# Performance work log

Hardware: AMD Instinct MI355X
Metric: run time of the kernel (lower is better)

Reference implementation:

```python
import jax, jax.numpy as jnp
import numpy as np

NUM_USERS = 100000
NUM_ITEMS = 50000
N_NODES = NUM_USERS + NUM_ITEMS
LATENT_DIM = 64
N_LAYERS = 3
N_EDGES = 4800000


def setup_inputs() -> dict:
    key = jax.random.key(0)
    ks = jax.random.split(key, 7)
    user_emb = jax.random.normal(ks[0], (NUM_USERS, LATENT_DIM), dtype=jnp.float32) * 0.1
    item_emb = jax.random.normal(ks[1], (NUM_ITEMS, LATENT_DIM), dtype=jnp.float32) * 0.1
    edge_src = jax.random.randint(ks[2], (N_EDGES,), 0, N_NODES, dtype=jnp.int32)
    edge_dst = jax.random.randint(ks[3], (N_EDGES,), 0, N_NODES, dtype=jnp.int32)
    # normalized adjacency values (positive, ~1/deg scale)
    edge_vals = jax.random.uniform(ks[4], (N_EDGES,), dtype=jnp.float32) * 0.05
    users = jax.random.randint(ks[5], (1024,), 0, NUM_USERS, dtype=jnp.int32)
    items = jax.random.randint(ks[6], (20000,), 0, NUM_ITEMS, dtype=jnp.int32)
    return {"user_emb": user_emb, "item_emb": item_emb,
            "edge_src": edge_src, "edge_dst": edge_dst, "edge_vals": edge_vals,
            "users": users, "items": items}


def _spmm(edge_src, edge_dst, edge_vals, x):
    # y[dst] += vals * x[src]  == sparse.mm(Graph, x)
    msgs = edge_vals[:, None] * x[edge_src]           # [E, D]
    return jax.ops.segment_sum(msgs, edge_dst, num_segments=N_NODES)


def reference(user_emb, item_emb, edge_src, edge_dst, edge_vals, users, items):
    all_em = jnp.concatenate([user_emb, item_emb], axis=0)  # [N, D]
    acc = all_em  # running sum over layers (mean at the end)
    h = all_em
    for _ in range(N_LAYERS):
        h = _spmm(edge_src, edge_dst, edge_vals, h)
        acc = acc + h
    result = acc / jnp.float32(N_LAYERS + 1)  # mean over stacked layers
    all_users = result[:NUM_USERS]
    all_items = result[NUM_USERS:]
    u = all_users[users]        # [Bu, D]
    it = all_items[items]       # [Bi, D]
    ratings = jax.nn.sigmoid(jnp.matmul(u, it.T))  # [Bu, Bi]
    return ratings
```

## Files before the change

### kernel.cpp

```cpp
#include <hip/hip_runtime.h>
#include <hip/hip_bf16.h>

#define NUM_USERS 100000
#define NUM_ITEMS 50000
#define N_NODES   150000
#define DIM       64
#define N_LAYERS  3
#define N_QU      1024
#define N_QI      20000
#define N_QTOT    (N_QU + N_QI)
#define SLOTS     80

#define BIN_SHIFT 9
#define BIN_W     512
#define NBINS     ((N_NODES + BIN_W - 1) >> BIN_SHIFT)
#define BIN_CAP   17472
#define S1_BATCH  4096

typedef __attribute__((ext_vector_type(8))) short bf16x8;
typedef __attribute__((ext_vector_type(4))) float f32x4;
typedef __attribute__((ext_vector_type(8))) unsigned short u16x8;

__device__ __forceinline__ short f2bf(float x) {
    unsigned u = __float_as_uint(x);
    u += 0x7FFF + ((u >> 16) & 1);
    return (short)(u >> 16);
}
__device__ __forceinline__ float bf2f(unsigned short u) {
    return __uint_as_float((unsigned)u << 16);
}

__global__ void init_h0(const float* __restrict__ ue, const float* __restrict__ ie,
                        unsigned short* __restrict__ h0) {
    const size_t n8   = (size_t)N_NODES * DIM / 8;
    const size_t uend = (size_t)NUM_USERS * DIM / 8;
    size_t stride = (size_t)gridDim.x * blockDim.x;
    for (size_t i = (size_t)blockIdx.x * blockDim.x + threadIdx.x; i < n8; i += stride) {
        const float4* s = (i < uend) ? ((const float4*)ue) + i * 2
                                     : ((const float4*)ie) + (i - uend) * 2;
        float4 a = s[0], b = s[1];
        ushort4 lo, hi;
        lo.x = (unsigned short)f2bf(a.x); lo.y = (unsigned short)f2bf(a.y);
        lo.z = (unsigned short)f2bf(a.z); lo.w = (unsigned short)f2bf(a.w);
        hi.x = (unsigned short)f2bf(b.x); hi.y = (unsigned short)f2bf(b.y);
        hi.z = (unsigned short)f2bf(b.z); hi.w = (unsigned short)f2bf(b.w);
        ((ushort4*)h0)[i * 2]     = lo;
        ((ushort4*)h0)[i * 2 + 1] = hi;
    }
}

__global__ void build_qlist(const int* __restrict__ users, const int* __restrict__ items,
                            int* __restrict__ qlist) {
    int i = blockIdx.x * blockDim.x + threadIdx.x;
    if (i < N_QU) qlist[i] = users[i];
    else if (i < N_QTOT) qlist[i] = NUM_USERS + items[i - N_QU];
}

__global__ __launch_bounds__(256) void s1_coarse(
        const int* __restrict__ src, const int* __restrict__ dst,
        const float* __restrict__ vals, int* __restrict__ gcnt,
        int2* __restrict__ binned, int n) {
    __shared__ int2 staging[S1_BATCH];
    __shared__ int  hist[NBINS];
    __shared__ int  base[NBINS];
    __shared__ int  pfx[NBINS];
    __shared__ int  part[256];
    const int t  = threadIdx.x;
    const int b0 = blockIdx.x * S1_BATCH;
    const int n4 = n >> 2;
    const int i4base = b0 >> 2;
    const int4*   d4 = (const int4*)dst;
    const int4*   s4 = (const int4*)src;
    const float4* v4 = (const float4*)vals;

    for (int i = t; i < NBINS; i += 256) hist[i] = 0;
    __syncthreads();

    #pragma unroll
    for (int k = 0; k < 4; ++k) {
        int i4 = i4base + k * 256 + t;
        if (i4 < n4) {
            int4 d = d4[i4];
            atomicAdd(&hist[d.x >> BIN_SHIFT], 1);
            atomicAdd(&hist[d.y >> BIN_SHIFT], 1);
            atomicAdd(&hist[d.z >> BIN_SHIFT], 1);
            atomicAdd(&hist[d.w >> BIN_SHIFT], 1);
        }
    }
    for (int e = (n & ~3) + t; e < n; e += 256)
        if (e >= b0 && e < b0 + S1_BATCH)
            atomicAdd(&hist[dst[e] >> BIN_SHIFT], 1);
    __syncthreads();

    {
        int i0 = 2 * t, i1 = 2 * t + 1;
        int h0v = (i0 < NBINS) ? hist[i0] : 0;
        int h1v = (i1 < NBINS) ? hist[i1] : 0;
        int s = h0v + h1v;
        part[t] = s;
        __syncthreads();
        int x = s;
        for (int off = 1; off < 256; off <<= 1) {
            int y = (t >= off) ? part[t - off] : 0;
            __syncthreads();
            x += y;
            part[t] = x;
            __syncthreads();
        }
        int exc = x - s;
        if (i0 < NBINS) pfx[i0] = exc;
        if (i1 < NBINS) pfx[i1] = exc + h0v;
    }
    __syncthreads();

    for (int i = t; i < NBINS; i += 256) {
        int c = hist[i];
        base[i] = (c > 0) ? atomicAdd(&gcnt[i], c) : 0;
    }
    __syncthreads();
    for (int i = t; i < NBINS; i += 256) hist[i] = 0;
    __syncthreads();

    #pragma unroll
    for (int k = 0; k < 4; ++k) {
        int i4 = i4base + k * 256 + t;
        if (i4 < n4) {
            int4   d = d4[i4];
            int4   s = s4[i4];
            float4 v = v4[i4];
            int bin, loc;
            bin = d.x >> BIN_SHIFT; loc = atomicAdd(&hist[bin], 1);
            staging[pfx[bin] + loc] = make_int2(((d.x & (BIN_W-1)) << 18) | s.x, __float_as_int(v.x));
            bin = d.y >> BIN_SHIFT; loc = atomicAdd(&hist[bin], 1);
            staging[pfx[bin] + loc] = make_int2(((d.y & (BIN_W-1)) << 18) | s.y, __float_as_int(v.y));
            bin = d.z >> BIN_SHIFT; loc = atomicAdd(&hist[bin], 1);
            staging[pfx[bin] + loc] = make_int2(((d.z & (BIN_W-1)) << 18) | s.z, __float_as_int(v.z));
            bin = d.w >> BIN_SHIFT; loc = atomicAdd(&hist[bin], 1);
            staging[pfx[bin] + loc] = make_int2(((d.w & (BIN_W-1)) << 18) | s.w, __float_as_int(v.w));
        }
    }
    for (int e = (n & ~3) + t; e < n; e += 256)
        if (e >= b0 && e < b0 + S1_BATCH) {
            int d = dst[e];
            int bin = d >> BIN_SHIFT;
            int loc = atomicAdd(&hist[bin], 1);
            staging[pfx[bin] + loc] = make_int2(((d & (BIN_W-1)) << 18) | src[e], __float_as_int(vals[e]));
        }
    __syncthreads();

    {
        int wid = t >> 6, lane = t & 63;
        for (int bin = wid; bin < NBINS; bin += 4) {
            int c = hist[bin];
            int g = base[bin];
            int p = pfx[bin];
            for (int l = lane; l < c; l += 64) {
                int slot = g + l;
                if (slot < BIN_CAP)
                    binned[(size_t)bin * BIN_CAP + slot] = staging[p + l];
            }
        }
    }
}

__global__ __launch_bounds__(1024) void s2_fine(
        const int* __restrict__ gcnt, const int2* __restrict__ binned,
        int* __restrict__ cnt, int2* __restrict__ buckets) {
    __shared__ int cursor[BIN_W];
    const int bin = blockIdx.x;
    const int t   = threadIdx.x;
    if (t < BIN_W) cursor[t] = 0;
    __syncthreads();

    int m = gcnt[bin]; if (m > BIN_CAP) m = BIN_CAP;
    const int2* bp = &binned[(size_t)bin * BIN_CAP];
    for (int i = t; i < m; i += 1024) {
        int2 p  = bp[i];
        int  dl = ((unsigned)p.x) >> 18;
        int  local = atomicAdd(&cursor[dl], 1);
        if (local < SLOTS) {
            int node = (bin << BIN_SHIFT) + dl;
            buckets[(size_t)node * SLOTS + local] =
                make_int2(p.x & 0x3FFFF, p.y);
        }
    }
    __syncthreads();

    if (t < BIN_W) {
        int node = (bin << BIN_SHIFT) + t;
        if (node < N_NODES) {
            int c = cursor[t]; if (c > SLOTS) c = SLOTS;
            cnt[node] = c;
        }
    }
}

__global__ __launch_bounds__(256) void spmm_bucket_bf16(
        const int* __restrict__ cnt, const int2* __restrict__ buckets,
        const unsigned short* __restrict__ x, unsigned short* __restrict__ y,
        const int* __restrict__ list, int count) {
    int lane8   = threadIdx.x & 7;
    int group   = (int)((blockIdx.x * blockDim.x + threadIdx.x) >> 3);
    int ngroups = (int)((gridDim.x * blockDim.x) >> 3);
    const u16x8* x8 = (const u16x8*)x;

    int i = group;
    if (i >= count) return;
    int node_n = list ? list[i] : i;
    int m_n = cnt[node_n];

    for (; i < count; i += ngroups) {
        int node = node_n;
        int m = m_n; if (m > SLOTS) m = SLOTS;
        int j = i + ngroups;
        if (j < count) { node_n = list ? list[j] : j; m_n = cnt[node_n]; }

        const int2* row  = &buckets[(size_t)node * SLOTS];
        const int4* row2 = (const int4*)row;
        float r[8];
        #pragma unroll
        for (int k = 0; k < 8; ++k) r[k] = 0.0f;

        int e = 0;
        for (; e + 4 <= m; e += 4) {
            int4 pa = row2[(e >> 1)];
            int4 pb = row2[(e >> 1) + 1];
            u16x8 x0 = x8[(size_t)pa.x * 8 + lane8];
            u16x8 x1 = x8[(size_t)pa.z * 8 + lane8];
            u16x8 x2 = x8[(size_t)pb.x * 8 + lane8];
            u16x8 x3 = x8[(size_t)pb.z * 8 + lane8];
            float v0 = __int_as_float(pa.y), v1 = __int_as_float(pa.w);
            float v2 = __int_as_float(pb.y), v3 = __int_as_float(pb.w);
            #pragma unroll
            for (int k = 0; k < 8; ++k) r[k] += v0 * bf2f(x0[k]);
            #pragma unroll
            for (int k = 0; k < 8; ++k) r[k] += v1 * bf2f(x1[k]);
            #pragma unroll
            for (int k = 0; k < 8; ++k) r[k] += v2 * bf2f(x2[k]);
            #pragma unroll
            for (int k = 0; k < 8; ++k) r[k] += v3 * bf2f(x3[k]);
        }
        if (e + 2 <= m) {
            int4 pa = row2[(e >> 1)];
            u16x8 x0 = x8[(size_t)pa.x * 8 + lane8];
            u16x8 x1 = x8[(size_t)pa.z * 8 + lane8];
            float v0 = __int_as_float(pa.y), v1 = __int_as_float(pa.w);
            #pragma unroll
            for (int k = 0; k < 8; ++k) r[k] += v0 * bf2f(x0[k]);
            #pragma unroll
            for (int k = 0; k < 8; ++k) r[k] += v1 * bf2f(x1[k]);
            e += 2;
        }
        if (e < m) {
            int2 p = row[e];
            float v = __int_as_float(p.y);
            u16x8 x0 = x8[(size_t)p.x * 8 + lane8];
            #pragma unroll
            for (int k = 0; k < 8; ++k) r[k] += v * bf2f(x0[k]);
        }

        u16x8 o;
        #pragma unroll
        for (int k = 0; k < 8; ++k) o[k] = (unsigned short)f2bf(r[k]);
        ((u16x8*)y)[(size_t)node * 8 + lane8] = o;
    }
}

__global__ __launch_bounds__(256) void prep_packed(
        const float* __restrict__ ue, const float* __restrict__ ie,
        const unsigned short* __restrict__ h1, const unsigned short* __restrict__ h2,
        const unsigned short* __restrict__ h3, const int* __restrict__ users,
        const int* __restrict__ items, unsigned short* __restrict__ packed) {
    int idx = blockIdx.x * blockDim.x + threadIdx.x;
    if (idx >= N_QTOT * 8) return;
    int q = idx >> 3, lane = idx & 7;

    const float* e0;
    size_t hoff;
    if (q < N_QU) {
        int u = users[q];
        e0   = &ue[(size_t)u * DIM];
        hoff = (size_t)u * DIM;
    } else {
        int it = items[q - N_QU];
        e0   = &ie[(size_t)it * DIM];
        hoff = (size_t)(NUM_USERS + it) * DIM;
    }
    int d0 = lane * 8;
    const float4* s0 = (const float4*)&e0[d0];
    float4 a0 = s0[0], a1 = s0[1];
    u16x8 b1 = *(const u16x8*)&h1[hoff + d0];
    u16x8 b2 = *(const u16x8*)&h2[hoff + d0];
    u16x8 b3 = *(const u16x8*)&h3[hoff + d0];

    float v[8];
    v[0] = a0.x; v[1] = a0.y; v[2] = a0.z; v[3] = a0.w;
    v[4] = a1.x; v[5] = a1.y; v[6] = a1.z; v[7] = a1.w;
    u16x8 o;
    #pragma unroll
    for (int k = 0; k < 8; ++k) {
        float t = (v[k] + bf2f(b1[k]) + bf2f(b2[k]) + bf2f(b3[k])) * 0.25f;
        o[k] = (unsigned short)f2bf(t);
    }
    *(u16x8*)&packed[(size_t)q * DIM + d0] = o;
}

__global__ __launch_bounds__(256) void rating_mfma(
        const unsigned short* __restrict__ packed, float* __restrict__ out) {
    __shared__ short Ut[64 * 72];
    __shared__ short Tt[256 * 72];
    const int bj = blockIdx.x;
    const int bi = blockIdx.y;
    const int tid = threadIdx.x;

    {
        int r = tid >> 2, c16 = (tid & 3) * 16;
        const bf16x8* s = (const bf16x8*)&packed[(size_t)(bi * 64 + r) * DIM + c16];
        *(bf16x8*)&Ut[r * 72 + c16]     = s[0];
        *(bf16x8*)&Ut[r * 72 + c16 + 8] = s[1];
    }

    #pragma unroll
    for (int p = 0; p < 4; ++p) {
        int r = (tid >> 2) + p * 64, c16 = (tid & 3) * 16;
        int jg = bj * 256 + r;
        bf16x8 lo = (bf16x8)(short)0, hi = (bf16x8)(short)0;
        if (jg < N_QI) {
            const bf16x8* s = (const bf16x8*)&packed[(size_t)(N_QU + jg) * DIM + c16];
            lo = s[0]; hi = s[1];
        }
        *(bf16x8*)&Tt[r * 72 + c16]     = lo;
        *(bf16x8*)&Tt[r * 72 + c16 + 8] = hi;
    }
    __syncthreads();

    const int wv = tid >> 6, lane = tid & 63;
    const int lr = lane & 15, kq = lane >> 4;

    f32x4 c[4][4];
    #pragma unroll
    for (int mr = 0; mr < 4; ++mr)
        #pragma unroll
        for (int nr = 0; nr < 4; ++nr)
            c[mr][nr] = (f32x4)(0.0f);

    #pragma unroll
    for (int kb = 0; kb < 2; ++kb) {
        bf16x8 a[4], b[4];
        #pragma unroll
        for (int mr = 0; mr < 4; ++mr)
            a[mr] = *(const bf16x8*)&Ut[(mr * 16 + lr) * 72 + (kb * 4 + kq) * 8];
        #pragma unroll
        for (int nr = 0; nr < 4; ++nr)
            b[nr] = *(const bf16x8*)&Tt[(wv * 64 + nr * 16 + lr) * 72 + (kb * 4 + kq) * 8];
        #pragma unroll
        for (int mr = 0; mr < 4; ++mr)
            #pragma unroll
            for (int nr = 0; nr < 4; ++nr)
                c[mr][nr] = __builtin_amdgcn_mfma_f32_16x16x32_bf16(a[mr], b[nr], c[mr][nr], 0, 0, 0);
    }

    #pragma unroll
    for (int mr = 0; mr < 4; ++mr) {
        int rowg = bi * 64 + mr * 16 + kq * 4;
        #pragma unroll
        for (int nr = 0; nr < 4; ++nr) {
            int colg = bj * 256 + wv * 64 + nr * 16 + lr;
            if (colg < N_QI) {
                #pragma unroll
                for (int q = 0; q < 4; ++q) {
                    float z = c[mr][nr][q];
                    out[(size_t)(rowg + q) * N_QI + colg] = 1.0f / (1.0f + __expf(-z));
                }
            }
        }
    }
}

extern "C" void kernel_launch(void* const* d_in, const int* in_sizes, int n_in,
                              void* d_out, int out_size, void* d_ws, size_t ws_size,
                              hipStream_t stream) {
    const float* user_emb  = (const float*)d_in[0];
    const float* item_emb  = (const float*)d_in[1];
    const int*   edge_src  = (const int*)d_in[2];
    const int*   edge_dst  = (const int*)d_in[3];
    const float* edge_vals = (const float*)d_in[4];
    const int*   users     = (const int*)d_in[5];
    const int*   items     = (const int*)d_in[6];
    float*       out       = (float*)d_out;
    int n_edges = in_sizes[2];

    const size_t nodeElems = (size_t)N_NODES * DIM;

    unsigned short* h0 = (unsigned short*)d_ws;
    unsigned short* h1 = h0 + nodeElems;
    unsigned short* h2 = h1 + nodeElems;
    unsigned short* h3 = h2 + nodeElems;
    int*  cnt     = (int*)(h3 + nodeElems);
    int2* buckets = (int2*)(cnt + N_NODES);
    int*  qlist   = (int*)(buckets + (size_t)N_NODES * SLOTS);
    unsigned short* packed = (unsigned short*)(qlist + N_QTOT);
    int*  gcnt    = (int*)(packed + (size_t)N_QTOT * DIM);
    int2* binned  = (int2*)h1;

    (void)hipMemsetAsync(gcnt, 0, NBINS * sizeof(int), stream);
    init_h0<<<2048, 256, 0, stream>>>(user_emb, item_emb, h0);
    build_qlist<<<(N_QTOT + 255) / 256, 256, 0, stream>>>(users, items, qlist);

    int nbatches = (n_edges + S1_BATCH - 1) / S1_BATCH;
    s1_coarse<<<nbatches, 256, 0, stream>>>(edge_src, edge_dst, edge_vals,
                                            gcnt, binned, n_edges);
    s2_fine<<<NBINS, 1024, 0, stream>>>(gcnt, binned, cnt, buckets);

    spmm_bucket_bf16<<<2048, 256, 0, stream>>>(cnt, buckets, h0, h1, nullptr, N_NODES);
    spmm_bucket_bf16<<<2048, 256, 0, stream>>>(cnt, buckets, h1, h2, nullptr, N_NODES);
    spmm_bucket_bf16<<<2048, 256, 0, stream>>>(cnt, buckets, h2, h3, qlist, N_QTOT);

    prep_packed<<<(N_QTOT * 8 + 255) / 256, 256, 0, stream>>>(
        user_emb, item_emb, h1, h2, h3, users, items, packed);

    dim3 grid((N_QI + 255) / 256, N_QU / 64);
    rating_mfma<<<grid, 256, 0, stream>>>(packed, out);
}
```

Before: 360.7 us.

## Split SpMM by source-node range into two cache-friendlier passes per layer

Edges in each node's bucket are now partitioned by source index around a pivot: low sources fill from the front and high sources from the back. The low and high counts are packed into one word. Each layer runs two SpMM passes, each gathering from only half of the input embedding table, so the random-gather working set is smaller and more likely to stay in cache. The cost is an extra kernel launch per layer, a read-modify-write of the output in the second pass, and a second bf16 rounding of partial sums.

```diff
diff --git a/kernel.cpp b/kernel.cpp
--- a/kernel.cpp
+++ b/kernel.cpp
@@ -10,6 +10,7 @@
 #define N_QI      20000
 #define N_QTOT    (N_QU + N_QI)
 #define SLOTS     80
+#define PIVOT     75000
 
 #define BIN_SHIFT 9
 #define BIN_W     512
@@ -166,10 +167,11 @@
 __global__ __launch_bounds__(1024) void s2_fine(
         const int* __restrict__ gcnt, const int2* __restrict__ binned,
         int* __restrict__ cnt, int2* __restrict__ buckets) {
-    __shared__ int cursor[BIN_W];
+    __shared__ int cur_lo[BIN_W];
+    __shared__ int cur_hi[BIN_W];
     const int bin = blockIdx.x;
     const int t   = threadIdx.x;
-    if (t < BIN_W) cursor[t] = 0;
+    if (t < BIN_W) { cur_lo[t] = 0; cur_hi[t] = 0; }
     __syncthreads();
 
     int m = gcnt[bin]; if (m > BIN_CAP) m = BIN_CAP;
@@ -177,11 +179,16 @@
     for (int i = t; i < m; i += 1024) {
         int2 p  = bp[i];
         int  dl = ((unsigned)p.x) >> 18;
-        int  local = atomicAdd(&cursor[dl], 1);
-        if (local < SLOTS) {
-            int node = (bin << BIN_SHIFT) + dl;
-            buckets[(size_t)node * SLOTS + local] =
-                make_int2(p.x & 0x3FFFF, p.y);
+        int  s  = p.x & 0x3FFFF;
+        int  node = (bin << BIN_SHIFT) + dl;
+        if (s < PIVOT) {
+            int loc = atomicAdd(&cur_lo[dl], 1);
+            if (loc < SLOTS)
+                buckets[(size_t)node * SLOTS + loc] = make_int2(s, p.y);
+        } else {
+            int loc = atomicAdd(&cur_hi[dl], 1);
+            if (loc < SLOTS)
+                buckets[(size_t)node * SLOTS + (SLOTS - 1 - loc)] = make_int2(s, p.y);
         }
     }
     __syncthreads();
@@ -189,16 +196,18 @@
     if (t < BIN_W) {
         int node = (bin << BIN_SHIFT) + t;
         if (node < N_NODES) {
-            int c = cursor[t]; if (c > SLOTS) c = SLOTS;
-            cnt[node] = c;
-        }
-    }
-}
-
-__global__ __launch_bounds__(256) void spmm_bucket_bf16(
+            int cl = cur_lo[t]; if (cl > SLOTS) cl = SLOTS;
+            int ch = cur_hi[t]; if (ch > SLOTS) ch = SLOTS;
+            if (cl + ch > SLOTS) ch = SLOTS - cl;
+            cnt[node] = cl | (ch << 16);
+        }
+    }
+}
+
+__global__ __launch_bounds__(256) void spmm_half(
         const int* __restrict__ cnt, const int2* __restrict__ buckets,
         const unsigned short* __restrict__ x, unsigned short* __restrict__ y,
-        const int* __restrict__ list, int count) {
+        const int* __restrict__ list, int count, int phase) {
     int lane8   = threadIdx.x & 7;
     int group   = (int)((blockIdx.x * blockDim.x + threadIdx.x) >> 3);
     int ngroups = (int)((gridDim.x * blockDim.x) >> 3);
@@ -207,22 +216,45 @@
     int i = group;
     if (i >= count) return;
     int node_n = list ? list[i] : i;
-    int m_n = cnt[node_n];
+    int c_n = cnt[node_n];
 
     for (; i < count; i += ngroups) {
         int node = node_n;
-        int m = m_n; if (m > SLOTS) m = SLOTS;
+        int c = c_n;
         int j = i + ngroups;
-        if (j < count) { node_n = list ? list[j] : j; m_n = cnt[node_n]; }
+        if (j < count) { node_n = list ? list[j] : j; c_n = cnt[node_n]; }
+
+        int beg, end;
+        if (phase == 0) {
+            beg = 0;
+            end = c & 0xFFFF; if (end > SLOTS) end = SLOTS;
+        } else {
+            int ch = ((unsigned)c) >> 16; if (ch > SLOTS) ch = SLOTS;
+            beg = SLOTS - ch; end = SLOTS;
+        }
 
         const int2* row  = &buckets[(size_t)node * SLOTS];
         const int4* row2 = (const int4*)row;
         float r[8];
-        #pragma unroll
-        for (int k = 0; k < 8; ++k) r[k] = 0.0f;
-
-        int e = 0;
-        for (; e + 4 <= m; e += 4) {
+        if (phase == 0) {
+            #pragma unroll
+            for (int k = 0; k < 8; ++k) r[k] = 0.0f;
+        } else {
+            u16x8 yv = ((const u16x8*)y)[(size_t)node * 8 + lane8];
+            #pragma unroll
+            for (int k = 0; k < 8; ++k) r[k] = bf2f(yv[k]);
+        }
+
+        int e = beg;
+        if ((e & 1) && e < end) {
+            int2 p = row[e];
+            float v = __int_as_float(p.y);
+            u16x8 x0 = x8[(size_t)p.x * 8 + lane8];
+            #pragma unroll
+            for (int k = 0; k < 8; ++k) r[k] += v * bf2f(x0[k]);
+            ++e;
+        }
+        for (; e + 4 <= end; e += 4) {
             int4 pa = row2[(e >> 1)];
             int4 pb = row2[(e >> 1) + 1];
             u16x8 x0 = x8[(size_t)pa.x * 8 + lane8];
@@ -240,7 +272,7 @@
             #pragma unroll
             for (int k = 0; k < 8; ++k) r[k] += v3 * bf2f(x3[k]);
         }
-        if (e + 2 <= m) {
+        if (e + 2 <= end) {
             int4 pa = row2[(e >> 1)];
             u16x8 x0 = x8[(size_t)pa.x * 8 + lane8];
             u16x8 x1 = x8[(size_t)pa.z * 8 + lane8];
@@ -251,7 +283,7 @@
             for (int k = 0; k < 8; ++k) r[k] += v1 * bf2f(x1[k]);
             e += 2;
         }
-        if (e < m) {
+        if (e < end) {
             int2 p = row[e];
             float v = __int_as_float(p.y);
             u16x8 x0 = x8[(size_t)p.x * 8 + lane8];
@@ -412,9 +444,13 @@
                                             gcnt, binned, n_edges);
     s2_fine<<<NBINS, 1024, 0, stream>>>(gcnt, binned, cnt, buckets);
 
-    spmm_bucket_bf16<<<2048, 256, 0, stream>>>(cnt, buckets, h0, h1, nullptr, N_NODES);
-    spmm_bucket_bf16<<<2048, 256, 0, stream>>>(cnt, buckets, h1, h2, nullptr, N_NODES);
-    spmm_bucket_bf16<<<2048, 256, 0, stream>>>(cnt, buckets, h2, h3, qlist, N_QTOT);
+    unsigned short* hs[4] = { h0, h1, h2, h3 };
+    for (int l = 0; l < N_LAYERS; ++l) {
+        const int* list = (l == N_LAYERS - 1) ? qlist : nullptr;
+        int count = (l == N_LAYERS - 1) ? N_QTOT : N_NODES;
+        spmm_half<<<2048, 256, 0, stream>>>(cnt, buckets, hs[l], hs[l + 1], list, count, 0);
+        spmm_half<<<2048, 256, 0, stream>>>(cnt, buckets, hs[l], hs[l + 1], list, count, 1);
+    }
 
     prep_packed<<<(N_QTOT * 8 + 255) / 256, 256, 0, stream>>>(
         user_emb, item_emb, h1, h2, h3, users, items, packed);
```

Result: slower. 382.0 us (+5.9%).
